# Performance work log

Measured on AMD Instinct MI355X. Metric: run time of the kernel, lower is better.

## Reference

```python
import jax, jax.numpy as jnp
import numpy as np

U = I = 100000  # user/item vocab (set equal; __init__ swaps them anyway)
P = 50          # position_len
D = 64          # hidden_units_u == hidden_units_i
B = 8192        # batch
H = 50          # history length


def _attn(data, key, W, b):
    # data: [B,D], key: [B,H,D]; Linear(2D,1) -> Tanh -> Softmax over H
    attn_in = jnp.concatenate([jnp.broadcast_to(data[:, None, :], key.shape), key], axis=-1)  # [B,H,2D]
    w = jax.nn.softmax(jnp.tanh(attn_in @ W + b), axis=1)  # [B,H,1]
    return jnp.sum(w * key, axis=1)  # [B,D]


def setup_inputs() -> dict:
    key = jax.random.key(0)
    ks = jax.random.split(key, 24)
    emb = lambda i, shape: jax.random.normal(ks[i], shape, jnp.float32) * 0.05
    uni = lambda i, shape: jax.random.uniform(ks[i], shape, jnp.float32, -1.0, 1.0)
    ri = lambda i, shape, hi: jax.random.randint(ks[i], shape, 0, hi, jnp.int32)
    return {
        "user1": ri(0, (B,), U), "item1": ri(1, (B,), I),
        "user2": ri(2, (B,), U), "item2": ri(3, (B,), I),
        "u_his": ri(4, (B, H), I), "u_pos": ri(5, (B, H), P), "u_his_mask": ri(6, (B, H), 2),
        "i_his": ri(7, (B, H), U), "i_pos": ri(8, (B, H), P), "i_his_mask": ri(9, (B, H), 2),
        "user1_emb": emb(10, (U, D)), "item1_emb": emb(11, (I, D)),
        "user1_bias": uni(12, (U,)), "item1_bias": uni(13, (I,)),
        "u_pos_emb": emb(14, (P, D)),
        "user2_emb": emb(15, (U, D)), "item2_emb": emb(16, (I, D)),
        "user2_bias": uni(17, (U,)), "item2_bias": uni(18, (I,)),
        "i_pos_emb": emb(19, (P, D)),
        "attn_u_W": emb(20, (2 * D, 1)), "attn_u_b": emb(21, (1,)),
        "attn_i_W": emb(22, (2 * D, 1)), "attn_i_b": emb(23, (1,)),
    }


def _forward(user1_emb, item1_emb, user1_bias, item1_bias, u_pos_emb,
             user2_emb, item2_emb, user2_bias, item2_bias, i_pos_emb,
             attn_u_W, attn_u_b, attn_i_W, attn_i_b,
             user1, item1, user2, item2,
             u_his, u_pos, u_his_mask, i_his, i_pos, i_his_mask):
    sg = jax.lax.stop_gradient
    mu = (u_his_mask != 0).astype(jnp.float32)[..., None]  # [B,H,1]
    mi = (i_his_mask != 0).astype(jnp.float32)[..., None]

    # branch 1 (shared-sign s, detached r)
    u1s = user1_emb[user1]; i1s = item1_emb[item1]
    u1s_b = user1_bias[user1]; i1s_b = item1_bias[item1]
    u1r = sg(user2_emb[user1]); i1r = sg(item2_emb[item1])
    u1r_b = sg(user2_bias[user1]); i1r_b = sg(item2_bias[item1])
    u_hiss = item1_emb[u_his] * mu            # [B,H,D], masked-zero
    i_hisr = sg(user2_emb[i_his]) * mi
    u_poss = u_pos_emb[u_pos] * mu
    i_posr = sg(i_pos_emb[i_pos]) * mi
    u_ds = _attn(i1s, u_hiss + u_poss, attn_u_W, attn_u_b)
    i_dr = _attn(u1r, i_hisr + i_posr, attn_i_W, attn_i_b)
    logits_us = u1s_b + i1s_b + jnp.sum((u_ds + i1s) * u1s, axis=1)
    logits_ir = u1r_b + i1r_b + jnp.sum((i_dr + i1r) * u1r, axis=1)

    # branch 2 (roles swapped)
    u2s = user2_emb[user2]; i2s = item2_emb[item2]
    u2s_b = user2_bias[user2]; i2s_b = item2_bias[item2]
    u2r = sg(user1_emb[user2]); i2r = sg(item1_emb[item2])
    u2r_b = sg(user1_bias[user2]); i2r_b = sg(item1_bias[item2])
    u_hisr = sg(item1_emb[u_his]) * mu
    i_hiss = user2_emb[i_his] * mi
    u_posr = sg(u_pos_emb[u_pos]) * mu
    i_poss = i_pos_emb[i_pos] * mi
    u_dr = _attn(i1r, u_hisr + u_posr, attn_u_W, attn_u_b)
    i_ds = _attn(u1s, i_hiss + i_poss, attn_i_W, attn_i_b)
    logits_ur = u2r_b + i2r_b + jnp.sum((u_dr + i2r) * u2r, axis=1)
    logits_is = u2s_b + i2s_b + jnp.sum((i_ds + i2s) * u2s, axis=1)

    loss_reg1 = jnp.sum(u1s ** 2) + jnp.sum(i1s ** 2) + jnp.sum(u_hiss ** 2)
    loss_reg2 = jnp.sum(u2s ** 2) + jnp.sum(i2s ** 2) + jnp.sum(i_hiss ** 2)
    return (logits_us, logits_ir, logits_ur, logits_is, loss_reg1, loss_reg2)


def reference(user1, item1, user2, item2, u_his, u_pos, u_his_mask, i_his, i_pos, i_his_mask,
              user1_emb, item1_emb, user1_bias, item1_bias, u_pos_emb,
              user2_emb, item2_emb, user2_bias, item2_bias, i_pos_emb,
              attn_u_W, attn_u_b, attn_i_W, attn_i_b):
    return _forward(user1_emb, item1_emb, user1_bias, item1_bias, u_pos_emb,
                    user2_emb, item2_emb, user2_bias, item2_bias, i_pos_emb,
                    attn_u_W, attn_u_b, attn_i_W, attn_i_b,
                    user1, item1, user2, item2,
                    u_his, u_pos, u_his_mask, i_his, i_pos, i_his_mask)
```

## Files before the change

### kernel.cpp

```cpp
#include <hip/hip_runtime.h>

#define NB 8192
#define NH 50
#define ND 64

__device__ __forceinline__ float wsum(float v) {
#pragma unroll
    for (int o = 32; o > 0; o >>= 1) v += __shfl_xor(v, o, 64);
    return v;
}

__device__ __forceinline__ float tanh_fast(float x) {
    const float e = __expf(2.0f * x);
    return (e - 1.0f) * __builtin_amdgcn_rcpf(e + 1.0f);
}

__global__ __launch_bounds__(256, 8) void kw_kernel(
    const float* __restrict__ t0, const float* __restrict__ t1,
    const float* __restrict__ t2, const float* __restrict__ t3,
    const float* __restrict__ w0, const float* __restrict__ w1,
    const float* __restrict__ w2, const float* __restrict__ w3,
    float* __restrict__ o0, float* __restrict__ o1,
    float* __restrict__ o2, float* __restrict__ o3,
    int r0, int r1, int r2, int r3,
    int b1, int b2, int b3)
{
    const int blk = blockIdx.x;
    const float* tab; const float* W; float* o; int rows, base;
    if (blk < b1)      { tab = t0; W = w0; o = o0; rows = r0; base = blk; }
    else if (blk < b2) { tab = t1; W = w1; o = o1; rows = r1; base = blk - b1; }
    else if (blk < b3) { tab = t2; W = w2; o = o2; rows = r2; base = blk - b2; }
    else               { tab = t3; W = w3; o = o3; rows = r3; base = blk - b3; }
    const int lane = threadIdx.x & 63;
    const int wv = threadIdx.x >> 6;
    const int sub = lane >> 4, j = lane & 15;
    const int row = base * 16 + wv * 4 + sub;
    const int rowc = min(row, rows - 1);
    const float4 v = *(const float4*)(tab + (size_t)rowc * ND + j * 4);
    const float4 w = *(const float4*)(W + j * 4);
    float p = v.x * w.x + v.y * w.y + v.z * w.z + v.w * w.w;
    p += __shfl_xor(p, 1, 64);
    p += __shfl_xor(p, 2, 64);
    p += __shfl_xor(p, 4, 64);
    p += __shfl_xor(p, 8, 64);
    if (j == 0 && row < rows) o[row] = p;
}

__global__ __launch_bounds__(256, 8) void fwd_kernel(
    const int* __restrict__ user1, const int* __restrict__ item1,
    const int* __restrict__ user2, const int* __restrict__ item2,
    const int* __restrict__ u_his, const int* __restrict__ u_pos, const int* __restrict__ u_mask,
    const int* __restrict__ i_his, const int* __restrict__ i_pos, const int* __restrict__ i_mask,
    const float* __restrict__ user1_emb, const float* __restrict__ item1_emb,
    const float* __restrict__ user1_bias, const float* __restrict__ item1_bias,
    const float* __restrict__ u_pos_emb,
    const float* __restrict__ user2_emb, const float* __restrict__ item2_emb,
    const float* __restrict__ user2_bias, const float* __restrict__ item2_bias,
    const float* __restrict__ i_pos_emb,
    const float* __restrict__ attn_u_W, const float* __restrict__ attn_u_b,
    const float* __restrict__ attn_i_W, const float* __restrict__ attn_i_b,
    const float* __restrict__ KWu, const float* __restrict__ KWi,
    const float* __restrict__ PWu, const float* __restrict__ PWi,
    float* __restrict__ out, float* __restrict__ ws)
{
    const int wave = threadIdx.x >> 6;
    const int d = threadIdx.x & 63;
    const int b = __builtin_amdgcn_readfirstlane(blockIdx.x * 2 + (wave >> 1));
    const bool iw = (wave & 1);

    const int iu1 = user1[b], ii1 = item1[b], iu2 = user2[b], ii2 = item2[b];

    const int*   his  = iw ? i_his  : u_his;
    const int*   posa = iw ? i_pos  : u_pos;
    const int*   msk  = iw ? i_mask : u_mask;
    const float* ktab = iw ? user2_emb : item1_emb;
    const float* ptab = iw ? i_pos_emb : u_pos_emb;
    const float* W    = iw ? attn_i_W  : attn_u_W;
    const float  bb   = iw ? attn_i_b[0] : attn_u_b[0];
    const float* KW   = iw ? KWi : KWu;
    const float* PW   = iw ? PWi : PWu;

    const float* qa_tab = iw ? user2_emb : item1_emb;
    const float* qb_tab = iw ? user1_emb : item2_emb;
    const int    qidx   = iw ? iu1 : ii1;
    const float qa = qa_tab[(size_t)qidx * ND + d];
    const float qb = qb_tab[(size_t)qidx * ND + d];
    const float Wq = W[d];
    const float cq_a = wsum(qa * Wq) + bb;
    const float cq_b = wsum(qb * Wq) + bb;
    const float e0_a = __expf(tanh_fast(cq_a));
    const float e0_b = __expf(tanh_fast(cq_b));

    int hidx = 0, hpos = 0;
    bool act = false;
    if (d < NH) {
        hidx = his[b * NH + d];
        hpos = posa[b * NH + d];
        act  = (msk[b * NH + d] != 0);
    }
    const float s = KW[hidx] + PW[hpos];
    float e_a = 0.0f, e_b = 0.0f;
    if (d < NH) {
        e_a = act ? __expf(tanh_fast(cq_a + s)) : e0_a;
        e_b = act ? __expf(tanh_fast(cq_b + s)) : e0_b;
    }
    const float den_a = wsum(e_a);
    const float den_b = wsum(e_b);

    const unsigned long long bal = __ballot(act);
    const int nact = __builtin_amdgcn_readfirstlane(__popcll(bal));
    const int below = __builtin_amdgcn_mbcnt_hi(
        (unsigned)(bal >> 32), __builtin_amdgcn_mbcnt_lo((unsigned)bal, 0));
    const int tgt = (act ? below : 63) << 2;
    const int idx_c = __builtin_amdgcn_ds_permute(tgt, hidx);
    const int pos_c = __builtin_amdgcn_ds_permute(tgt, hpos);
    const int ea_c  = __builtin_amdgcn_ds_permute(tgt, __float_as_int(e_a));
    const int eb_c  = __builtin_amdgcn_ds_permute(tgt, __float_as_int(e_b));

    float o_a = 0.0f, o_b = 0.0f, reg = 0.0f;
#pragma unroll 4
    for (int h = 0; h < nact; ++h) {
        const int ih = __builtin_amdgcn_readlane(idx_c, h);
        const int ip = __builtin_amdgcn_readlane(pos_c, h);
        const float ea = __int_as_float(__builtin_amdgcn_readlane(ea_c, h));
        const float eb = __int_as_float(__builtin_amdgcn_readlane(eb_c, h));
        const float kv = ktab[(size_t)ih * ND + d];
        const float pv = ptab[ip * ND + d];
        const float k = kv + pv;
        o_a += ea * k;
        o_b += eb * k;
        reg += kv * kv;
    }
    o_a *= __builtin_amdgcn_rcpf(den_a);
    o_b *= __builtin_amdgcn_rcpf(den_b);

    const float pa = iw ? item2_emb[(size_t)ii1 * ND + d] : user1_emb[(size_t)iu1 * ND + d];
    const float add_a = iw ? pa : qa;
    const float mul_a = iw ? qa : pa;
    const float add_b = (iw ? item2_emb : item1_emb)[(size_t)ii2 * ND + d];
    const float mul_b = (iw ? user2_emb : user1_emb)[(size_t)iu2 * ND + d];

    const float l_a = wsum((o_a + add_a) * mul_a);
    const float l_b = wsum((o_b + add_b) * mul_b);
    const float rv = iw ? (mul_b * mul_b + add_b * add_b) : (mul_a * mul_a + qa * qa);
    const float r = wsum(rv + reg);

    const float* ub = iw ? user2_bias : user1_bias;
    const float* ib = iw ? item2_bias : item1_bias;
    if (d == 0) {
        out[(iw ? NB : 0) + b]          = ub[iu1] + ib[ii1] + l_a;
        out[(iw ? 3 * NB : 2 * NB) + b] = ub[iu2] + ib[ii2] + l_b;
        ws[(iw ? NB : 0) + b] = r;
    }
}

__global__ __launch_bounds__(256, 8) void fwd_fallback(
    const int* __restrict__ user1, const int* __restrict__ item1,
    const int* __restrict__ user2, const int* __restrict__ item2,
    const int* __restrict__ u_his, const int* __restrict__ u_pos, const int* __restrict__ u_mask,
    const int* __restrict__ i_his, const int* __restrict__ i_pos, const int* __restrict__ i_mask,
    const float* __restrict__ user1_emb, const float* __restrict__ item1_emb,
    const float* __restrict__ user1_bias, const float* __restrict__ item1_bias,
    const float* __restrict__ u_pos_emb,
    const float* __restrict__ user2_emb, const float* __restrict__ item2_emb,
    const float* __restrict__ user2_bias, const float* __restrict__ item2_bias,
    const float* __restrict__ i_pos_emb,
    const float* __restrict__ attn_u_W, const float* __restrict__ attn_u_b,
    const float* __restrict__ attn_i_W, const float* __restrict__ attn_i_b,
    float* __restrict__ out, float* __restrict__ ws)
{
    const int wave = threadIdx.x >> 6;
    const int d = threadIdx.x & 63;
    const int b = __builtin_amdgcn_readfirstlane(blockIdx.x * 2 + (wave >> 1));
    const bool iw = (wave & 1);

    const int iu1 = user1[b], ii1 = item1[b], iu2 = user2[b], ii2 = item2[b];
    const int*   his  = iw ? i_his  : u_his;
    const int*   posa = iw ? i_pos  : u_pos;
    const int*   msk  = iw ? i_mask : u_mask;
    const float* ktab = iw ? user2_emb : item1_emb;
    const float* ptab = iw ? i_pos_emb : u_pos_emb;
    const float* W    = iw ? attn_i_W  : attn_u_W;
    const float  bb   = iw ? attn_i_b[0] : attn_u_b[0];
    const float* qa_tab = iw ? user2_emb : item1_emb;
    const float* qb_tab = iw ? user1_emb : item2_emb;
    const int    qidx   = iw ? iu1 : ii1;
    const float qa = qa_tab[(size_t)qidx * ND + d];
    const float qb = qb_tab[(size_t)qidx * ND + d];
    const float Wq = W[d], Wk = W[ND + d];
    const float cq_a = wsum(qa * Wq) + bb;
    const float cq_b = wsum(qb * Wq) + bb;

    int hidx = 0, hpos = 0;
    bool act = false;
    if (d < NH) {
        hidx = his[b * NH + d];
        hpos = posa[b * NH + d];
        act  = (msk[b * NH + d] != 0);
    }
    const unsigned long long bal = __ballot(act);
    const int nact = __builtin_amdgcn_readfirstlane(__popcll(bal));
    const int below = __builtin_amdgcn_mbcnt_hi(
        (unsigned)(bal >> 32), __builtin_amdgcn_mbcnt_lo((unsigned)bal, 0));
    const int tgt = (act ? below : 63) << 2;
    const int idx_c = __builtin_amdgcn_ds_permute(tgt, hidx);
    const int pos_c = __builtin_amdgcn_ds_permute(tgt, hpos);

    float o_a = 0.0f, o_b = 0.0f, den_a = 0.0f, den_b = 0.0f, reg = 0.0f;
#pragma unroll 4
    for (int h = 0; h < nact; ++h) {
        const int ih = __builtin_amdgcn_readlane(idx_c, h);
        const int ip = __builtin_amdgcn_readlane(pos_c, h);
        const float kv = ktab[(size_t)ih * ND + d];
        const float pv = ptab[(size_t)ip * ND + d];
        const float k = kv + pv;
        reg += kv * kv;
        const float s = wsum(k * Wk);
        const float ea = __expf(tanh_fast(cq_a + s));
        const float eb = __expf(tanh_fast(cq_b + s));
        o_a += ea * k;  den_a += ea;
        o_b += eb * k;  den_b += eb;
    }
    den_a += (float)(NH - nact) * __expf(tanh_fast(cq_a));
    den_b += (float)(NH - nact) * __expf(tanh_fast(cq_b));
    o_a *= __builtin_amdgcn_rcpf(den_a);
    o_b *= __builtin_amdgcn_rcpf(den_b);

    const float pa = iw ? item2_emb[(size_t)ii1 * ND + d] : user1_emb[(size_t)iu1 * ND + d];
    const float add_a = iw ? pa : qa;
    const float mul_a = iw ? qa : pa;
    const float add_b = (iw ? item2_emb : item1_emb)[(size_t)ii2 * ND + d];
    const float mul_b = (iw ? user2_emb : user1_emb)[(size_t)iu2 * ND + d];
    const float l_a = wsum((o_a + add_a) * mul_a);
    const float l_b = wsum((o_b + add_b) * mul_b);
    const float rv = iw ? (mul_b * mul_b + add_b * add_b) : (mul_a * mul_a + qa * qa);
    const float r = wsum(rv + reg);
    const float* ub = iw ? user2_bias : user1_bias;
    const float* ib = iw ? item2_bias : item1_bias;
    if (d == 0) {
        out[(iw ? NB : 0) + b]          = ub[iu1] + ib[ii1] + l_a;
        out[(iw ? 3 * NB : 2 * NB) + b] = ub[iu2] + ib[ii2] + l_b;
        ws[(iw ? NB : 0) + b] = r;
    }
}

__global__ void reduce_kernel(const float* __restrict__ ws, float* __restrict__ out) {
    float a = 0.0f, c = 0.0f;
    for (int i = threadIdx.x; i < NB; i += 256) {
        a += ws[i];
        c += ws[NB + i];
    }
    a = wsum(a);
    c = wsum(c);
    __shared__ float sa[4], sc[4];
    const int w = threadIdx.x >> 6, d = threadIdx.x & 63;
    if (d == 0) { sa[w] = a; sc[w] = c; }
    __syncthreads();
    if (threadIdx.x == 0) {
        out[4 * NB]     = sa[0] + sa[1] + sa[2] + sa[3];
        out[4 * NB + 1] = sc[0] + sc[1] + sc[2] + sc[3];
    }
}

extern "C" void kernel_launch(void* const* d_in, const int* in_sizes, int n_in,
                              void* d_out, int out_size, void* d_ws, size_t ws_size,
                              hipStream_t stream) {
    const int* user1 = (const int*)d_in[0];
    const int* item1 = (const int*)d_in[1];
    const int* user2 = (const int*)d_in[2];
    const int* item2 = (const int*)d_in[3];
    const int* u_his = (const int*)d_in[4];
    const int* u_pos = (const int*)d_in[5];
    const int* u_msk = (const int*)d_in[6];
    const int* i_his = (const int*)d_in[7];
    const int* i_pos = (const int*)d_in[8];
    const int* i_msk = (const int*)d_in[9];
    const float* user1_emb  = (const float*)d_in[10];
    const float* item1_emb  = (const float*)d_in[11];
    const float* user1_bias = (const float*)d_in[12];
    const float* item1_bias = (const float*)d_in[13];
    const float* u_pos_emb  = (const float*)d_in[14];
    const float* user2_emb  = (const float*)d_in[15];
    const float* item2_emb  = (const float*)d_in[16];
    const float* user2_bias = (const float*)d_in[17];
    const float* item2_bias = (const float*)d_in[18];
    const float* i_pos_emb  = (const float*)d_in[19];
    const float* attn_u_W = (const float*)d_in[20];
    const float* attn_u_b = (const float*)d_in[21];
    const float* attn_i_W = (const float*)d_in[22];
    const float* attn_i_b = (const float*)d_in[23];
    float* out = (float*)d_out;
    float* ws  = (float*)d_ws;

    const int I_rows = in_sizes[11] / ND;
    const int U_rows = in_sizes[15] / ND;
    const int P_rows = in_sizes[14] / ND;

    float* KWu = ws + 2 * NB;
    float* KWi = KWu + I_rows;
    float* PWu = KWi + U_rows;
    float* PWi = PWu + 64;
    const size_t need = (size_t)(2 * NB + I_rows + U_rows + 128) * sizeof(float);

    if (ws_size >= need) {
        const int nb0 = (I_rows + 15) / 16;
        const int nb1 = (U_rows + 15) / 16;
        const int nb2 = (P_rows + 15) / 16;
        const int b1 = nb0, b2 = nb0 + nb1, b3 = nb0 + nb1 + nb2;
        const int total = b3 + nb2;
        kw_kernel<<<total, 256, 0, stream>>>(
            item1_emb, user2_emb, u_pos_emb, i_pos_emb,
            attn_u_W + ND, attn_i_W + ND, attn_u_W + ND, attn_i_W + ND,
            KWu, KWi, PWu, PWi,
            I_rows, U_rows, P_rows, P_rows,
            b1, b2, b3);
        fwd_kernel<<<NB / 2, 256, 0, stream>>>(
            user1, item1, user2, item2,
            u_his, u_pos, u_msk, i_his, i_pos, i_msk,
            user1_emb, item1_emb, user1_bias, item1_bias, u_pos_emb,
            user2_emb, item2_emb, user2_bias, item2_bias, i_pos_emb,
            attn_u_W, attn_u_b, attn_i_W, attn_i_b,
            KWu, KWi, PWu, PWi,
            out, ws);
    } else {
        fwd_fallback<<<NB / 2, 256, 0, stream>>>(
            user1, item1, user2, item2,
            u_his, u_pos, u_msk, i_his, i_pos, i_msk,
            user1_emb, item1_emb, user1_bias, item1_bias, u_pos_emb,
            user2_emb, item2_emb, user2_bias, item2_bias, i_pos_emb,
            attn_u_W, attn_u_b, attn_i_W, attn_i_b,
            out, ws);
    }
    reduce_kernel<<<1, 256, 0, stream>>>(ws, out);
}
```

Before: 207.8 us.

## Batch history gathers in groups of 16 and replace reduce kernel with atomics

The history loop is restructured so 16 lane indices are read first, then 16 independent embedding loads are issued together, then accumulated. This raises memory-level parallelism for the latency-bound gathers, at the cost of more registers and padded work on partial groups. The separate regularisation reduce kernel is removed: each block adds its partial sums to the output tail with atomicAdd, and the tail is zeroed by the preceding kernel. Tail-row embedding loads are also hoisted ahead of the loop so their latency overlaps it.

New measurement: 274.4 us. 32.0% more time.

```diff
diff --git a/kernel.cpp b/kernel.cpp
--- a/kernel.cpp
+++ b/kernel.cpp
@@ -23,8 +23,13 @@
     float* __restrict__ o0, float* __restrict__ o1,
     float* __restrict__ o2, float* __restrict__ o3,
     int r0, int r1, int r2, int r3,
-    int b1, int b2, int b3)
+    int b1, int b2, int b3,
+    float* __restrict__ out)
 {
+    if (blockIdx.x == 0 && threadIdx.x == 0) {
+        out[4 * NB] = 0.0f;
+        out[4 * NB + 1] = 0.0f;
+    }
     const int blk = blockIdx.x;
     const float* tab; const float* W; float* o; int rows, base;
     if (blk < b1)      { tab = t0; W = w0; o = o0; rows = r0; base = blk; }
@@ -61,7 +66,7 @@
     const float* __restrict__ attn_i_W, const float* __restrict__ attn_i_b,
     const float* __restrict__ KWu, const float* __restrict__ KWi,
     const float* __restrict__ PWu, const float* __restrict__ PWi,
-    float* __restrict__ out, float* __restrict__ ws)
+    float* __restrict__ out)
 {
     const int wave = threadIdx.x >> 6;
     const int d = threadIdx.x & 63;
@@ -85,6 +90,11 @@
     const int    qidx   = iw ? iu1 : ii1;
     const float qa = qa_tab[(size_t)qidx * ND + d];
     const float qb = qb_tab[(size_t)qidx * ND + d];
+
+    const float pa    = iw ? item2_emb[(size_t)ii1 * ND + d] : user1_emb[(size_t)iu1 * ND + d];
+    const float add_b = (iw ? item2_emb : item1_emb)[(size_t)ii2 * ND + d];
+    const float mul_b = (iw ? user2_emb : user1_emb)[(size_t)iu2 * ND + d];
+
     const float Wq = W[d];
     const float cq_a = wsum(qa * Wq) + bb;
     const float cq_b = wsum(qb * Wq) + bb;
@@ -118,28 +128,39 @@
     const int eb_c  = __builtin_amdgcn_ds_permute(tgt, __float_as_int(e_b));
 
     float o_a = 0.0f, o_b = 0.0f, reg = 0.0f;
-#pragma unroll 4
-    for (int h = 0; h < nact; ++h) {
-        const int ih = __builtin_amdgcn_readlane(idx_c, h);
-        const int ip = __builtin_amdgcn_readlane(pos_c, h);
-        const float ea = __int_as_float(__builtin_amdgcn_readlane(ea_c, h));
-        const float eb = __int_as_float(__builtin_amdgcn_readlane(eb_c, h));
-        const float kv = ktab[(size_t)ih * ND + d];
-        const float pv = ptab[ip * ND + d];
-        const float k = kv + pv;
-        o_a += ea * k;
-        o_b += eb * k;
-        reg += kv * kv;
+    const int nact16 = (nact + 15) & ~15;
+    for (int base = 0; base < nact16; base += 16) {
+        int ihs[16], ips[16];
+#pragma unroll
+        for (int j = 0; j < 16; ++j) {
+            const int hc = min(base + j, nact - 1);
+            ihs[j] = __builtin_amdgcn_readlane(idx_c, hc);
+            ips[j] = __builtin_amdgcn_readlane(pos_c, hc);
+        }
+        float kvs[16], pvs[16];
+#pragma unroll
+        for (int j = 0; j < 16; ++j) {
+            kvs[j] = ktab[(size_t)ihs[j] * ND + d];
+            pvs[j] = ptab[ips[j] * ND + d];
+        }
+#pragma unroll
+        for (int j = 0; j < 16; ++j) {
+            const int hh = base + j;
+            const int hc = min(hh, nact - 1);
+            const bool v = hh < nact;
+            const float ea = v ? __int_as_float(__builtin_amdgcn_readlane(ea_c, hc)) : 0.0f;
+            const float eb = v ? __int_as_float(__builtin_amdgcn_readlane(eb_c, hc)) : 0.0f;
+            const float k = kvs[j] + pvs[j];
+            o_a += ea * k;
+            o_b += eb * k;
+            reg += v ? kvs[j] * kvs[j] : 0.0f;
+        }
     }
     o_a *= __builtin_amdgcn_rcpf(den_a);
     o_b *= __builtin_amdgcn_rcpf(den_b);
 
-    const float pa = iw ? item2_emb[(size_t)ii1 * ND + d] : user1_emb[(size_t)iu1 * ND + d];
     const float add_a = iw ? pa : qa;
     const float mul_a = iw ? qa : pa;
-    const float add_b = (iw ? item2_emb : item1_emb)[(size_t)ii2 * ND + d];
-    const float mul_b = (iw ? user2_emb : user1_emb)[(size_t)iu2 * ND + d];
-
     const float l_a = wsum((o_a + add_a) * mul_a);
     const float l_b = wsum((o_b + add_b) * mul_b);
     const float rv = iw ? (mul_b * mul_b + add_b * add_b) : (mul_a * mul_a + qa * qa);
@@ -147,11 +168,20 @@
 
     const float* ub = iw ? user2_bias : user1_bias;
     const float* ib = iw ? item2_bias : item1_bias;
+    __shared__ float red[4];
     if (d == 0) {
         out[(iw ? NB : 0) + b]          = ub[iu1] + ib[ii1] + l_a;
         out[(iw ? 3 * NB : 2 * NB) + b] = ub[iu2] + ib[ii2] + l_b;
-        ws[(iw ? NB : 0) + b] = r;
-    }
+        red[wave] = r;
+    }
+    __syncthreads();
+    if (threadIdx.x == 0)  atomicAdd(&out[4 * NB],     red[0] + red[2]);
+    if (threadIdx.x == 64) atomicAdd(&out[4 * NB + 1], red[1] + red[3]);
+}
+
+__global__ void zero_tail_kernel(float* __restrict__ out) {
+    out[4 * NB] = 0.0f;
+    out[4 * NB + 1] = 0.0f;
 }
 
 __global__ __launch_bounds__(256, 8) void fwd_fallback(
@@ -167,7 +197,7 @@
     const float* __restrict__ i_pos_emb,
     const float* __restrict__ attn_u_W, const float* __restrict__ attn_u_b,
     const float* __restrict__ attn_i_W, const float* __restrict__ attn_i_b,
-    float* __restrict__ out, float* __restrict__ ws)
+    float* __restrict__ out)
 {
     const int wave = threadIdx.x >> 6;
     const int d = threadIdx.x & 63;
@@ -237,29 +267,15 @@
     const float r = wsum(rv + reg);
     const float* ub = iw ? user2_bias : user1_bias;
     const float* ib = iw ? item2_bias : item1_bias;
+    __shared__ float red[4];
     if (d == 0) {
         out[(iw ? NB : 0) + b]          = ub[iu1] + ib[ii1] + l_a;
         out[(iw ? 3 * NB : 2 * NB) + b] = ub[iu2] + ib[ii2] + l_b;
-        ws[(iw ? NB : 0) + b] = r;
-    }
-}
-
-__global__ void reduce_kernel(const float* __restrict__ ws, float* __restrict__ out) {
-    float a = 0.0f, c = 0.0f;
-    for (int i = threadIdx.x; i < NB; i += 256) {
-        a += ws[i];
-        c += ws[NB + i];
-    }
-    a = wsum(a);
-    c = wsum(c);
-    __shared__ float sa[4], sc[4];
-    const int w = threadIdx.x >> 6, d = threadIdx.x & 63;
-    if (d == 0) { sa[w] = a; sc[w] = c; }
+        red[wave] = r;
+    }
     __syncthreads();
-    if (threadIdx.x == 0) {
-        out[4 * NB]     = sa[0] + sa[1] + sa[2] + sa[3];
-        out[4 * NB + 1] = sc[0] + sc[1] + sc[2] + sc[3];
-    }
+    if (threadIdx.x == 0)  atomicAdd(&out[4 * NB],     red[0] + red[2]);
+    if (threadIdx.x == 64) atomicAdd(&out[4 * NB + 1], red[1] + red[3]);
 }
 
 extern "C" void kernel_launch(void* const* d_in, const int* in_sizes, int n_in,
@@ -296,11 +312,11 @@
     const int U_rows = in_sizes[15] / ND;
     const int P_rows = in_sizes[14] / ND;
 
-    float* KWu = ws + 2 * NB;
+    float* KWu = ws;
     float* KWi = KWu + I_rows;
     float* PWu = KWi + U_rows;
     float* PWi = PWu + 64;
-    const size_t need = (size_t)(2 * NB + I_rows + U_rows + 128) * sizeof(float);
+    const size_t need = (size_t)(I_rows + U_rows + 128) * sizeof(float);
 
     if (ws_size >= need) {
         const int nb0 = (I_rows + 15) / 16;
@@ -313,7 +329,7 @@
             attn_u_W + ND, attn_i_W + ND, attn_u_W + ND, attn_i_W + ND,
             KWu, KWi, PWu, PWi,
             I_rows, U_rows, P_rows, P_rows,
-            b1, b2, b3);
+            b1, b2, b3, out);
         fwd_kernel<<<NB / 2, 256, 0, stream>>>(
             user1, item1, user2, item2,
             u_his, u_pos, u_msk, i_his, i_pos, i_msk,
@@ -321,15 +337,15 @@
             user2_emb, item2_emb, user2_bias, item2_bias, i_pos_emb,
             attn_u_W, attn_u_b, attn_i_W, attn_i_b,
             KWu, KWi, PWu, PWi,
-            out, ws);
+            out);
     } else {
+        zero_tail_kernel<<<1, 1, 0, stream>>>(out);
         fwd_fallback<<<NB / 2, 256, 0, stream>>>(
             user1, item1, user2, item2,
             u_his, u_pos, u_msk, i_his, i_pos, i_msk,
             user1_emb, item1_emb, user1_bias, item1_bias, u_pos_emb,
             user2_emb, item2_emb, user2_bias, item2_bias, i_pos_emb,
             attn_u_W, attn_u_b, attn_i_W, attn_i_b,
-            out, ws);
-    }
-    reduce_kernel<<<1, 256, 0, stream>>>(ws, out);
-}
+            out);
+    }
+}
```

## Gather history rows with float4 loads, four history entries per wave iteration

Applied to the files above, without the earlier changes.

Restructures the attention gather loop so each wave processes four history entries at once. Each 16-lane group loads one 64-float row as float4s, replacing one scalar-per-lane row load per entry with readlane broadcasts. Per-entry indices and weights now come through ds_bpermute. The query/output dot products are recomputed as float4 partial dots scaled by 0.25 after full-wave sums, since each row is replicated across the four subgroups. Launch bounds are relaxed from 8 to 4 blocks per CU, which allows more registers per thread at the cost of occupancy.

Measured after the change: 203.1 us. 1.02x faster.

```diff
diff --git a/kernel.cpp b/kernel.cpp
--- a/kernel.cpp
+++ b/kernel.cpp
@@ -13,6 +13,10 @@
 __device__ __forceinline__ float tanh_fast(float x) {
     const float e = __expf(2.0f * x);
     return (e - 1.0f) * __builtin_amdgcn_rcpf(e + 1.0f);
+}
+
+__device__ __forceinline__ float dot4(const float4 a, const float4 b) {
+    return a.x * b.x + a.y * b.y + a.z * b.z + a.w * b.w;
 }
 
 __global__ __launch_bounds__(256, 8) void kw_kernel(
@@ -38,7 +42,7 @@
     const int rowc = min(row, rows - 1);
     const float4 v = *(const float4*)(tab + (size_t)rowc * ND + j * 4);
     const float4 w = *(const float4*)(W + j * 4);
-    float p = v.x * w.x + v.y * w.y + v.z * w.z + v.w * w.w;
+    float p = dot4(v, w);
     p += __shfl_xor(p, 1, 64);
     p += __shfl_xor(p, 2, 64);
     p += __shfl_xor(p, 4, 64);
@@ -46,7 +50,7 @@
     if (j == 0 && row < rows) o[row] = p;
 }
 
-__global__ __launch_bounds__(256, 8) void fwd_kernel(
+__global__ __launch_bounds__(256, 4) void fwd_kernel(
     const int* __restrict__ user1, const int* __restrict__ item1,
     const int* __restrict__ user2, const int* __restrict__ item2,
     const int* __restrict__ u_his, const int* __restrict__ u_pos, const int* __restrict__ u_mask,
@@ -67,6 +71,8 @@
     const int d = threadIdx.x & 63;
     const int b = __builtin_amdgcn_readfirstlane(blockIdx.x * 2 + (wave >> 1));
     const bool iw = (wave & 1);
+    const int sub = d >> 4;
+    const int col = (d & 15) * 4;
 
     const int iu1 = user1[b], ii1 = item1[b], iu2 = user2[b], ii2 = item2[b];
 
@@ -80,17 +86,6 @@
     const float* KW   = iw ? KWi : KWu;
     const float* PW   = iw ? PWi : PWu;
 
-    const float* qa_tab = iw ? user2_emb : item1_emb;
-    const float* qb_tab = iw ? user1_emb : item2_emb;
-    const int    qidx   = iw ? iu1 : ii1;
-    const float qa = qa_tab[(size_t)qidx * ND + d];
-    const float qb = qb_tab[(size_t)qidx * ND + d];
-    const float Wq = W[d];
-    const float cq_a = wsum(qa * Wq) + bb;
-    const float cq_b = wsum(qb * Wq) + bb;
-    const float e0_a = __expf(tanh_fast(cq_a));
-    const float e0_b = __expf(tanh_fast(cq_b));
-
     int hidx = 0, hpos = 0;
     bool act = false;
     if (d < NH) {
@@ -99,6 +94,23 @@
         act  = (msk[b * NH + d] != 0);
     }
     const float s = KW[hidx] + PW[hpos];
+
+    const float* qa_tab = iw ? user2_emb : item1_emb;
+    const float* qb_tab = iw ? user1_emb : item2_emb;
+    const int    qidx   = iw ? iu1 : ii1;
+    const float4 qa4 = *(const float4*)(qa_tab + (size_t)qidx * ND + col);
+    const float4 qb4 = *(const float4*)(qb_tab + (size_t)qidx * ND + col);
+    const float4 pa4 = *(const float4*)((iw ? item2_emb : user1_emb) +
+                                        (size_t)(iw ? ii1 : iu1) * ND + col);
+    const float4 ab4 = *(const float4*)((iw ? item2_emb : item1_emb) + (size_t)ii2 * ND + col);
+    const float4 mb4 = *(const float4*)((iw ? user2_emb : user1_emb) + (size_t)iu2 * ND + col);
+    const float4 Wq4 = *(const float4*)(W + col);
+
+    const float cq_a = wsum(dot4(qa4, Wq4)) * 0.25f + bb;
+    const float cq_b = wsum(dot4(qb4, Wq4)) * 0.25f + bb;
+    const float e0_a = __expf(tanh_fast(cq_a));
+    const float e0_b = __expf(tanh_fast(cq_b));
+
     float e_a = 0.0f, e_b = 0.0f;
     if (d < NH) {
         e_a = act ? __expf(tanh_fast(cq_a + s)) : e0_a;
@@ -117,33 +129,37 @@
     const int ea_c  = __builtin_amdgcn_ds_permute(tgt, __float_as_int(e_a));
     const int eb_c  = __builtin_amdgcn_ds_permute(tgt, __float_as_int(e_b));
 
-    float o_a = 0.0f, o_b = 0.0f, reg = 0.0f;
+    float4 oa = make_float4(0.f, 0.f, 0.f, 0.f);
+    float4 ob = make_float4(0.f, 0.f, 0.f, 0.f);
+    float reg = 0.0f;
 #pragma unroll 4
-    for (int h = 0; h < nact; ++h) {
-        const int ih = __builtin_amdgcn_readlane(idx_c, h);
-        const int ip = __builtin_amdgcn_readlane(pos_c, h);
-        const float ea = __int_as_float(__builtin_amdgcn_readlane(ea_c, h));
-        const float eb = __int_as_float(__builtin_amdgcn_readlane(eb_c, h));
-        const float kv = ktab[(size_t)ih * ND + d];
-        const float pv = ptab[ip * ND + d];
-        const float k = kv + pv;
-        o_a += ea * k;
-        o_b += eb * k;
-        reg += kv * kv;
-    }
-    o_a *= __builtin_amdgcn_rcpf(den_a);
-    o_b *= __builtin_amdgcn_rcpf(den_b);
-
-    const float pa = iw ? item2_emb[(size_t)ii1 * ND + d] : user1_emb[(size_t)iu1 * ND + d];
-    const float add_a = iw ? pa : qa;
-    const float mul_a = iw ? qa : pa;
-    const float add_b = (iw ? item2_emb : item1_emb)[(size_t)ii2 * ND + d];
-    const float mul_b = (iw ? user2_emb : user1_emb)[(size_t)iu2 * ND + d];
-
-    const float l_a = wsum((o_a + add_a) * mul_a);
-    const float l_b = wsum((o_b + add_b) * mul_b);
-    const float rv = iw ? (mul_b * mul_b + add_b * add_b) : (mul_a * mul_a + qa * qa);
-    const float r = wsum(rv + reg);
+    for (int base = 0; base < nact; base += 4) {
+        const int sid = base + sub;
+        const bool v = sid < nact;
+        const int off = (v ? sid : 0) << 2;
+        const int ih = __builtin_amdgcn_ds_bpermute(off, idx_c);
+        const int ip = __builtin_amdgcn_ds_bpermute(off, pos_c);
+        const float ea = v ? __int_as_float(__builtin_amdgcn_ds_bpermute(off, ea_c)) : 0.0f;
+        const float eb = v ? __int_as_float(__builtin_amdgcn_ds_bpermute(off, eb_c)) : 0.0f;
+        const float4 kv = *(const float4*)(ktab + (size_t)ih * ND + col);
+        const float4 pv = *(const float4*)(ptab + ip * ND + col);
+        float4 k;
+        k.x = kv.x + pv.x; k.y = kv.y + pv.y; k.z = kv.z + pv.z; k.w = kv.w + pv.w;
+        oa.x += ea * k.x; oa.y += ea * k.y; oa.z += ea * k.z; oa.w += ea * k.w;
+        ob.x += eb * k.x; ob.y += eb * k.y; ob.z += eb * k.z; ob.w += eb * k.w;
+        const float m = v ? 1.0f : 0.0f;
+        reg += m * dot4(kv, kv);
+    }
+
+    const float rd_a = __builtin_amdgcn_rcpf(den_a);
+    const float rd_b = __builtin_amdgcn_rcpf(den_b);
+    const float4 aa4 = iw ? pa4 : qa4;
+    const float4 ma4 = iw ? qa4 : pa4;
+    const float l_a = wsum(dot4(oa, ma4) * rd_a + 0.25f * dot4(aa4, ma4));
+    const float l_b = wsum(dot4(ob, mb4) * rd_b + 0.25f * dot4(ab4, mb4));
+    const float rv = iw ? (dot4(mb4, mb4) + dot4(ab4, ab4))
+                        : (dot4(ma4, ma4) + dot4(qa4, qa4));
+    const float r = wsum(reg + 0.25f * rv);
 
     const float* ub = iw ? user2_bias : user1_bias;
     const float* ib = iw ? item2_bias : item1_bias;
```
